# Kernel optimization log

Measured on AMD Instinct MI355X. Metric: run time of the kernel, lower is better.

Reference implementation:

```python
import jax, jax.numpy as jnp
import numpy as np
from jax import lax

B, L, D_MODEL = 4, 1024, 512
D_STATE, D_CONV, D_INNER = 16, 4, 2 * D_MODEL


def setup_inputs() -> dict:
    key = jax.random.key(0)
    ks = jax.random.split(key, 8)
    s = 0.02
    x = jax.random.normal(ks[0], (B, L, D_MODEL), dtype=jnp.float32)
    W_in = jax.random.normal(ks[1], (D_MODEL, 2 * D_INNER), dtype=jnp.float32) * s
    conv_w = jax.random.normal(ks[2], (D_INNER, 1, D_CONV), dtype=jnp.float32) * s  # OIH, depthwise
    conv_b = jnp.zeros((D_INNER,), jnp.float32)
    W_x = jax.random.normal(ks[3], (D_INNER, 2 * D_STATE), dtype=jnp.float32) * s
    W_dt = jax.random.normal(ks[4], (D_INNER, D_INNER), dtype=jnp.float32) * s
    b_dt = jnp.zeros((D_INNER,), jnp.float32)
    # A_log = -logspace(log10(0.001), log10(1.0), d_state); used directly as A in the scan
    A_log = -jnp.logspace(np.log10(1e-3), 0.0, D_STATE, dtype=jnp.float32)
    D_skip = jnp.ones((D_INNER,), jnp.float32) * 0.1
    W_out = jax.random.normal(ks[5], (D_INNER, D_MODEL), dtype=jnp.float32) * s
    gamma = jnp.ones((D_MODEL,), jnp.float32)
    beta = jnp.zeros((D_MODEL,), jnp.float32)
    return dict(x=x, W_in=W_in, conv_w=conv_w, conv_b=conv_b, W_x=W_x, W_dt=W_dt,
                b_dt=b_dt, A_log=A_log, D_skip=D_skip, W_out=W_out, gamma=gamma, beta=beta)


def _mamba_forward(x, W_in, conv_w, conv_b, W_x, W_dt, b_dt, A_log, D_skip, W_out, gamma, beta):
    x = jnp.clip(x, -10.0, 10.0)
    x_and_res = x @ W_in                                  # [B, L, 2*d_inner]
    xp, res = jnp.split(x_and_res, 2, axis=-1)
    # Depthwise causal conv1d: torch pads d_conv-1 both sides then slices [:L] -> left-pad only.
    xt = jnp.transpose(xp, (0, 2, 1))                     # [B, d_inner, L]
    xc = lax.conv_general_dilated(xt, conv_w, window_strides=(1,),
                                  padding=[(D_CONV - 1, 0)],
                                  dimension_numbers=('NCH', 'OIH', 'NCH'),
                                  feature_group_count=D_INNER)
    xc = xc + conv_b[None, :, None]
    xc = jax.nn.silu(jnp.transpose(xc, (0, 2, 1)))        # [B, L, d_inner]
    ssm = xc @ W_x                                        # [B, L, 2*d_state]
    Bm, Cm = jnp.split(ssm, 2, axis=-1)                   # each [B, L, d_state]
    delta = xc @ W_dt + b_dt                              # [B, L, d_inner] (no softplus in source)

    # Selective scan over time (sequential recurrence)
    def step(h, inp):
        u_t, d_t, B_t, C_t = inp                          # [B,I], [B,I], [B,S], [B,S]
        dA = jnp.exp(jnp.clip(d_t[:, :, None] * A_log, -5.0, 5.0))   # [B, I, S]
        h = dA * h + (d_t[:, :, None] * B_t[:, None, :]) * u_t[:, :, None]
        y = jnp.einsum('bis,bs->bi', h, C_t)
        return h, y

    tm = lambda a: jnp.swapaxes(a, 0, 1)                  # time-major
    h0 = jnp.zeros((x.shape[0], D_INNER, D_STATE), xc.dtype)
    _, ys = lax.scan(step, h0, (tm(xc), tm(delta), tm(Bm), tm(Cm)))
    y = jnp.swapaxes(ys, 0, 1) + xc * D_skip              # D skip connection

    y = y * jax.nn.silu(res)                              # gating
    out = y @ W_out
    r = out + x                                           # residual
    mu = jnp.mean(r, axis=-1, keepdims=True)
    var = jnp.var(r, axis=-1, keepdims=True)
    return gamma * (r - mu) / jnp.sqrt(var + 1e-5) + beta


def reference(x, W_in, conv_w, conv_b, W_x, W_dt, b_dt, A_log, D_skip, W_out, gamma, beta):
    return _mamba_forward(x, W_in, conv_w, conv_b, W_x, W_dt, b_dt, A_log, D_skip, W_out, gamma, beta)
```

## Files before the change

kernel.cpp:

```cpp
#include <hip/hip_runtime.h>
#include <hip/hip_bf16.h>

typedef __hip_bfloat16 bf16;
typedef unsigned short ushort_t;
typedef unsigned int uint_t;
typedef __attribute__((ext_vector_type(8))) __bf16 bf16x8;
typedef __attribute__((ext_vector_type(8))) ushort_t u16x8;
typedef __attribute__((ext_vector_type(4))) ushort_t u16x4;
typedef __attribute__((ext_vector_type(4))) float f32x4;

#define BB 4
#define LL 1024
#define DM 512
#define DS 16
#define DI 1024
#define ROWS 4096
#define NC 64
#define CT 16
#define NDTX 1152

#define CLP2 7.21347520f

__device__ __forceinline__ float b2f(bf16 v) { return __bfloat162float(v); }

__device__ __forceinline__ float load_flag(const void* src, int i, int isbf)
{
    return isbf ? b2f(((const bf16*)src)[i]) : ((const float*)src)[i];
}

__device__ __forceinline__ ushort_t f2b_bits(float v)
{
    bf16 t = __float2bfloat16(v);
    return *(ushort_t*)&t;
}

__device__ __forceinline__ float bits2f(ushort_t u)
{
    uint_t w = ((uint_t)u) << 16;
    return __uint_as_float(w);
}

__device__ __forceinline__ int detect_local(const ushort_t* wdt)
{
    __shared__ int bad;
    if (threadIdx.x == 0) bad = 0;
    __syncthreads();
    ushort_t u = wdt[threadIdx.x & 255];
    if (((u >> 7) & 0xFF) >= 127) atomicAdd(&bad, 1);
    __syncthreads();
    return (bad <= 8) ? 1 : 0;
}

__global__ __launch_bounds__(256)
void prep_all(const void* x, const void* Win, const void* Wdt, const void* Wx,
              const void* Wout, const void* cw, const void* cb, const void* Alog,
              const void* Dsk, const void* gam, const void* bet, const void* bdtin,
              bf16* __restrict__ xbf, bf16* __restrict__ WtIn,
              bf16* __restrict__ WtDtx, bf16* __restrict__ WtOut,
              float* __restrict__ ccw, float* __restrict__ ccb,
              float* __restrict__ cAlg, float* __restrict__ cDsk,
              float* __restrict__ cgam, float* __restrict__ cbet,
              float* __restrict__ bdtx)
{
    const int isbf = detect_local((const ushort_t*)Wdt);
    int blk = blockIdx.x;

    if (blk < 2048) {
        int idx = blk * 256 + threadIdx.x;
        float v[4];
        if (isbf) {
            uint2 raw = ((const uint2*)x)[idx];
            v[0] = __uint_as_float(raw.x << 16);
            v[1] = __uint_as_float(raw.x & 0xFFFF0000u);
            v[2] = __uint_as_float(raw.y << 16);
            v[3] = __uint_as_float(raw.y & 0xFFFF0000u);
        } else {
            float4 raw = ((const float4*)x)[idx];
            v[0] = raw.x; v[1] = raw.y; v[2] = raw.z; v[3] = raw.w;
        }
        uint_t b0, b1;
        b0 = f2b_bits(fminf(fmaxf(v[0], -10.f), 10.f))
           | ((uint_t)f2b_bits(fminf(fmaxf(v[1], -10.f), 10.f)) << 16);
        b1 = f2b_bits(fminf(fmaxf(v[2], -10.f), 10.f))
           | ((uint_t)f2b_bits(fminf(fmaxf(v[3], -10.f), 10.f)) << 16);
        uint2 ow; ow.x = b0; ow.y = b1;
        ((uint2*)xbf)[idx] = ow;
    } else if (blk < 4640) {
        int tb = blk - 2048;
        const void* src; bf16* dst; int K, Nsrc, tpr;
        if (tb < 1024)      { src = Win;  dst = WtIn;   K = 512;  Nsrc = 2048; tpr = 64; }
        else if (tb < 2048) { tb -= 1024; src = Wdt;  dst = WtDtx; K = 1024; Nsrc = 1024; tpr = 32; }
        else if (tb < 2080) { tb -= 2048; src = Wx;   dst = WtDtx + 1024 * 1024; K = 1024; Nsrc = 32; tpr = 1; }
        else                { tb -= 2080; src = Wout; dst = WtOut;  K = 1024; Nsrc = 512;  tpr = 16; }
        int k0 = (tb / tpr) * 32, n0 = (tb % tpr) * 32;

        __shared__ float tile[32][33];
        int tx = threadIdx.x & 31, ty = threadIdx.x >> 5;
        #pragma unroll
        for (int j = 0; j < 4; ++j)
            tile[ty + 8 * j][tx] = load_flag(src, (k0 + ty + 8 * j) * Nsrc + n0 + tx, isbf);
        __syncthreads();
        #pragma unroll
        for (int j = 0; j < 4; ++j)
            dst[(size_t)(n0 + ty + 8 * j) * K + k0 + tx] = __float2bfloat16(tile[tx][ty + 8 * j]);
    } else {
        int i = (blk - 4640) * 256 + threadIdx.x;
        if (i < 4096)        ccw[i] = load_flag(cw, i, isbf);
        else if (i < 5120)   ccb[i - 4096] = load_flag(cb, i - 4096, isbf);
        else if (i < 5136)   cAlg[i - 5120] = load_flag(Alog, i - 5120, isbf);
        else if (i < 6160)   cDsk[i - 5136] = load_flag(Dsk, i - 5136, isbf);
        else if (i < 6672)   cgam[i - 6160] = load_flag(gam, i - 6160, isbf);
        else if (i < 7184)   cbet[i - 6672] = load_flag(bet, i - 6672, isbf);
        else if (i < 8336) {
            int j = i - 7184;
            bdtx[j] = (j < DI) ? load_flag(bdtin, j, isbf) : 0.f;
        } else if (i < 106640) {
            (WtDtx + 1056 * 1024)[i - 8336] = __float2bfloat16(0.f);
        }
    }
}

__device__ __forceinline__ void gload16(const bf16* g, ushort_t* l)
{
    __builtin_amdgcn_global_load_lds(
        (const __attribute__((address_space(1))) void*)g,
        (__attribute__((address_space(3))) void*)l, 16, 0, 0);
}

template <int TM, int TN, bool OBF, bool OT, bool SPLIT>
__global__ __launch_bounds__(256)
void gemm_mfma(const bf16* __restrict__ A, const bf16* __restrict__ Bt,
               const float* __restrict__ bias, void* __restrict__ Cv,
               void* __restrict__ Cv2, int M, int N, int K)
{
    constexpr int MI = TM / 32, NJ = TN / 32;
    constexpr int NQA = TM * 8 / 256;
    constexpr int NQB = TN * 8 / 256;
    __shared__ ushort_t As[TM * 64];
    __shared__ ushort_t Bs[TN * 64];

    const int tid = threadIdx.x;
    const int lane = tid & 63;
    const int w = tid >> 6;
    const int wr = w >> 1, wc = w & 1;
    const int m0 = blockIdx.y * TM;
    const int n0 = blockIdx.x * TN;

    const bf16* gA[NQA]; ushort_t* lA[NQA];
    #pragma unroll
    for (int q = 0; q < NQA; ++q) {
        int p = q * 256 + tid;
        int row = p >> 3, kc = ((p & 7) - row) & 7;
        gA[q] = A + (size_t)(m0 + row) * K + kc * 8;
        lA[q] = &As[(q * 256 + w * 64) * 8];
    }
    const bf16* gB[NQB]; ushort_t* lB[NQB];
    #pragma unroll
    for (int q = 0; q < NQB; ++q) {
        int p = q * 256 + tid;
        int row = p >> 3, kc = ((p & 7) - row) & 7;
        gB[q] = Bt + (size_t)(n0 + row) * K + kc * 8;
        lB[q] = &Bs[(q * 256 + w * 64) * 8];
    }

    f32x4 acc[MI][NJ];
    #pragma unroll
    for (int i = 0; i < MI; ++i)
        #pragma unroll
        for (int j = 0; j < NJ; ++j)
            acc[i][j] = (f32x4){0.f, 0.f, 0.f, 0.f};

    const int ko = lane >> 4;
    const int ml = lane & 15;

    for (int k0 = 0; k0 < K; k0 += 64) {
        #pragma unroll
        for (int q = 0; q < NQA; ++q) gload16(gA[q] + k0, lA[q]);
        #pragma unroll
        for (int q = 0; q < NQB; ++q) gload16(gB[q] + k0, lB[q]);
        __syncthreads();

        #pragma unroll
        for (int half = 0; half < 2; ++half) {
            bf16x8 af[MI], bfr[NJ];
            #pragma unroll
            for (int i = 0; i < MI; ++i) {
                int m = wr * (TM / 2) + i * 16 + ml;
                af[i] = *(const bf16x8*)&As[(m * 8 + ((half * 4 + ko + m) & 7)) * 8];
            }
            #pragma unroll
            for (int j = 0; j < NJ; ++j) {
                int n = wc * (TN / 2) + j * 16 + ml;
                bfr[j] = *(const bf16x8*)&Bs[(n * 8 + ((half * 4 + ko + n) & 7)) * 8];
            }
            #pragma unroll
            for (int i = 0; i < MI; ++i)
                #pragma unroll
                for (int j = 0; j < NJ; ++j)
                    acc[i][j] = __builtin_amdgcn_mfma_f32_16x16x32_bf16(
                        af[i], bfr[j], acc[i][j], 0, 0, 0);
        }
        __syncthreads();
    }

    const int rq = lane >> 4;
    #pragma unroll
    for (int j = 0; j < NJ; ++j) {
        int n = n0 + wc * (TN / 2) + j * 16 + ml;
        float bv = bias ? bias[n] : 0.f;
        #pragma unroll
        for (int i = 0; i < MI; ++i) {
            int mb = m0 + wr * (TM / 2) + i * 16 + rq * 4;
            if (SPLIT && n >= 1024) {
                if (n < 1088) {
                    #pragma unroll
                    for (int r = 0; r < 4; ++r)
                        ((float*)Cv2)[(size_t)(mb + r) * 64 + (n - 1024)] =
                            acc[i][j][r] + bv;
                }
            } else if (OT) {
                u16x4 pk;
                #pragma unroll
                for (int r = 0; r < 4; ++r)
                    pk[r] = f2b_bits(acc[i][j][r] + bv);
                *(u16x4*)((ushort_t*)Cv + (size_t)n * M + mb) = pk;
            } else {
                #pragma unroll
                for (int r = 0; r < 4; ++r) {
                    float v = acc[i][j][r] + bv;
                    if (OBF) ((bf16*)Cv)[(size_t)(mb + r) * N + n] = __float2bfloat16(v);
                    else     ((float*)Cv)[(size_t)(mb + r) * N + n] = v;
                }
            }
        }
    }
}

__global__ __launch_bounds__(256)
void conv_silu(const bf16* __restrict__ xrbT, const float* __restrict__ cw,
               const float* __restrict__ cb, bf16* __restrict__ xcT,
               bf16* __restrict__ xc)
{
    __shared__ ushort_t tile[64 * 72];
    const int blk = blockIdx.x;
    const int ch0 = (blk & 15) * 64;
    const int T0b = (blk >> 4) * 64;
    const int lc = threadIdx.x >> 2, tg = threadIdx.x & 3;
    const int i = ch0 + lc;
    const int T0 = T0b + tg * 16;

    const ushort_t* base = (const ushort_t*)xrbT + (size_t)i * ROWS + T0;
    u16x8 m0 = *(const u16x8*)base;
    u16x8 m1 = *(const u16x8*)(base + 8);
    u16x8 pv = {0, 0, 0, 0, 0, 0, 0, 0};
    if ((T0 & (LL - 1)) != 0) pv = *(const u16x8*)(base - 8);

    float4 w = ((const float4*)cw)[i];
    float bs = cb[i];
    float xm3 = bits2f(pv[5]), xm2 = bits2f(pv[6]), xm1 = bits2f(pv[7]);
    u16x8 o0, o1;
    #pragma unroll
    for (int tt = 0; tt < 16; ++tt) {
        float x0 = bits2f(tt < 8 ? m0[tt] : m1[tt - 8]);
        float acc = bs;
        acc = fmaf(xm3, w.x, acc);
        acc = fmaf(xm2, w.y, acc);
        acc = fmaf(xm1, w.z, acc);
        acc = fmaf(x0,  w.w, acc);
        ushort_t ob = f2b_bits(acc / (1.f + __expf(-acc)));
        if (tt < 8) o0[tt] = ob; else o1[tt - 8] = ob;
        xm3 = xm2; xm2 = xm1; xm1 = x0;
    }
    ushort_t* dt = (ushort_t*)xcT + (size_t)i * ROWS + T0;
    *(u16x8*)dt = o0;
    *(u16x8*)(dt + 8) = o1;
    *(u16x8*)&tile[lc * 72 + tg * 16] = o0;
    *(u16x8*)&tile[lc * 72 + tg * 16 + 8] = o1;
    __syncthreads();
    const int lt = threadIdx.x >> 2, cg = threadIdx.x & 3;
    u16x8 q0, q1;
    #pragma unroll
    for (int j = 0; j < 8; ++j) q0[j] = tile[(cg * 16 + j) * 72 + lt];
    #pragma unroll
    for (int j = 8; j < 16; ++j) q1[j - 8] = tile[(cg * 16 + j) * 72 + lt];
    ushort_t* wp = (ushort_t*)xc + (size_t)(T0b + lt) * DI + ch0 + cg * 16;
    *(u16x8*)wp = q0;
    *(u16x8*)(wp + 8) = q1;
}

__global__ __launch_bounds__(1024)
void scan_fused(const bf16* __restrict__ xcT, const bf16* __restrict__ dT,
                const float* __restrict__ ssm, const bf16* __restrict__ xrbT,
                const float* __restrict__ A_log, const float* __restrict__ Dskip,
                bf16* __restrict__ ybf)
{
    __shared__ uint_t lsum[DS * NC * 16];

    const int tid = threadIdx.x;
    const int b = blockIdx.x >> 6;
    const int ch0 = (blockIdx.x & 63) << 4;
    const int chl = tid & 15;
    const int c = tid >> 4;
    const int i = ch0 + chl;
    const size_t tb = (size_t)b * LL + c * CT;

    float a2[DS];
    #pragma unroll
    for (int s = 0; s < DS; ++s) {
        uint_t bits = (uint_t)__builtin_amdgcn_readfirstlane((int)__float_as_uint(A_log[s]));
        a2[s] = __uint_as_float(bits) * 1.44269504f;
    }

    const u16x8* dp = (const u16x8*)((const ushort_t*)dT + (size_t)i * ROWS + tb);
    const u16x8* up = (const u16x8*)((const ushort_t*)xcT + (size_t)i * ROWS + tb);
    const u16x8* rp = (const u16x8*)((const ushort_t*)xrbT + (size_t)(1024 + i) * ROWS + tb);

    float h[DS] = {};
    float p[DS];
    #pragma unroll
    for (int s = 0; s < DS; ++s) p[s] = 1.f;

    #pragma unroll
    for (int half = 0; half < 2; ++half) {
        u16x8 dv8 = dp[half];
        u16x8 uv8 = up[half];
        #pragma unroll
        for (int t = 0; t < 8; ++t) {
            float dv = bits2f(dv8[t]);
            float uv = bits2f(uv8[t]);
            float du = dv * uv;
            const f32x4* sv = (const f32x4*)(ssm + (tb + half * 8 + t) * 64);
            #pragma unroll
            for (int g = 0; g < 4; ++g) {
                f32x4 Bq = sv[g];
                #pragma unroll
                for (int q = 0; q < 4; ++q) {
                    int s = g * 4 + q;
                    float e = fminf(fmaxf(dv * a2[s], -CLP2), CLP2);
                    float dA = exp2f(e);
                    h[s] = fmaf(dA, h[s], du * Bq[q]);
                    p[s] *= dA;
                }
            }
        }
    }
    #pragma unroll
    for (int s = 0; s < DS; ++s)
        lsum[s * 1024 + tid] = (uint_t)f2b_bits(p[s]) | ((uint_t)f2b_bits(h[s]) << 16);
    __syncthreads();

    if (tid < 256) {
        int cl = tid & 15, s = tid >> 4;
        float hh = 0.f;
        for (int cc = 0; cc < NC; ++cc) {
            int off = s * 1024 + cc * 16 + cl;
            uint_t wrd = lsum[off];
            float pp = bits2f((ushort_t)(wrd & 0xFFFF));
            float qq = bits2f((ushort_t)(wrd >> 16));
            lsum[off] = (uint_t)f2b_bits(hh);
            hh = fmaf(pp, hh, qq);
        }
    }
    __syncthreads();

    #pragma unroll
    for (int s = 0; s < DS; ++s) h[s] = bits2f((ushort_t)lsum[s * 1024 + tid]);

    const float dsk = Dskip[i];

    #pragma unroll
    for (int half = 0; half < 2; ++half) {
        u16x8 dv8 = dp[half];
        u16x8 uv8 = up[half];
        u16x8 rv8 = rp[half];
        #pragma unroll
        for (int t = 0; t < 8; ++t) {
            float dv = bits2f(dv8[t]);
            float uv = bits2f(uv8[t]);
            float du = dv * uv;
            const f32x4* sv = (const f32x4*)(ssm + (tb + half * 8 + t) * 64);
            float y = 0.f;
            #pragma unroll
            for (int g = 0; g < 4; ++g) {
                f32x4 Bq = sv[g];
                f32x4 Cq = sv[4 + g];
                #pragma unroll
                for (int q = 0; q < 4; ++q) {
                    int s = g * 4 + q;
                    float e = fminf(fmaxf(dv * a2[s], -CLP2), CLP2);
                    float dA = exp2f(e);
                    h[s] = fmaf(dA, h[s], du * Bq[q]);
                    y = fmaf(h[s], Cq[q], y);
                }
            }
            float res = bits2f(rv8[t]);
            float g2 = res / (1.f + __expf(-res));
            ybf[(tb + half * 8 + t) * DI + i] = __float2bfloat16((y + uv * dsk) * g2);
        }
    }
}

__global__ __launch_bounds__(256)
void ln_kernel(const bf16* __restrict__ outp, const void* __restrict__ xsrc,
               const void* __restrict__ wdt_probe,
               const float* __restrict__ gamma, const float* __restrict__ beta,
               void* __restrict__ out)
{
    const int isbf = detect_local((const ushort_t*)wdt_probe);
    const int row = blockIdx.x;
    const int tid = threadIdx.x;

    float r[2];
    float sum = 0.f, ss = 0.f;
    #pragma unroll
    for (int q = 0; q < 2; ++q) {
        int j = tid + q * 256;
        float xv = load_flag(xsrc, row * DM + j, isbf);
        xv = fminf(fmaxf(xv, -10.f), 10.f);
        float v = b2f(outp[(size_t)row * DM + j]) + xv;
        r[q] = v;
        sum += v;
        ss = fmaf(v, v, ss);
    }
    #pragma unroll
    for (int off = 32; off >= 1; off >>= 1) {
        sum += __shfl_down(sum, off);
        ss  += __shfl_down(ss, off);
    }
    __shared__ float s1[4], s2[4];
    __shared__ float stats[2];
    int wid = tid >> 6, lane = tid & 63;
    if (lane == 0) { s1[wid] = sum; s2[wid] = ss; }
    __syncthreads();
    if (tid == 0) {
        float S = s1[0] + s1[1] + s1[2] + s1[3];
        float Qq = s2[0] + s2[1] + s2[2] + s2[3];
        float mean = S / DM;
        float var = Qq / DM - mean * mean;
        stats[0] = mean;
        stats[1] = rsqrtf(var + 1e-5f);
    }
    __syncthreads();
    float mean = stats[0], rstd = stats[1];
    #pragma unroll
    for (int q = 0; q < 2; ++q) {
        int j = tid + q * 256;
        float v = (r[q] - mean) * rstd * gamma[j] + beta[j];
        size_t o = (size_t)row * DM + j;
        if (isbf) ((bf16*)out)[o] = __float2bfloat16(v);
        else      ((float*)out)[o] = v;
    }
}

extern "C" void kernel_launch(void* const* d_in, const int* in_sizes, int n_in,
                              void* d_out, int out_size, void* d_ws, size_t ws_size,
                              hipStream_t stream)
{
    float* W = (float*)d_ws;
    float* ccw  = W;
    float* ccb  = ccw  + 4096;
    float* cAlg = ccb  + 1024;
    float* cDsk = cAlg + 16;
    float* cgam = cDsk + 1024;
    float* cbet = cgam + 512;
    float* bdtx = cbet + 512;
    float* ssm  = bdtx + 1152;
    bf16*  xbf  = (bf16*)(ssm + 262144);
    bf16*  xrbT = xbf  + 2097152;
    bf16*  xcT  = xrbT + 8388608;
    bf16*  xc   = xcT  + 4194304;
    bf16*  ybf  = xc   + 4194304;
    bf16*  dT   = ybf  + 4194304;
    bf16*  outp = dT   + 4194304;
    bf16*  WtIn = outp + 2097152;
    bf16*  WtDtx= WtIn + 1048576;
    bf16*  WtOut= WtDtx+ 1179648;

    prep_all<<<5057, 256, 0, stream>>>(
        d_in[0], d_in[1], d_in[5], d_in[4], d_in[9], d_in[2], d_in[3],
        d_in[7], d_in[8], d_in[10], d_in[11], d_in[6],
        xbf, WtIn, WtDtx, WtOut, ccw, ccb, cAlg, cDsk, cgam, cbet, bdtx);

    gemm_mfma<128, 128, true, true, false><<<dim3(2048 / 128, ROWS / 128), 256, 0, stream>>>(
        xbf, WtIn, nullptr, xrbT, nullptr, ROWS, 2048, 512);

    conv_silu<<<1024, 256, 0, stream>>>(xrbT, ccw, ccb, xcT, xc);

    gemm_mfma<64, 128, true, true, true><<<dim3(NDTX / 128, ROWS / 64), 256, 0, stream>>>(
        xc, WtDtx, bdtx, dT, ssm, ROWS, NDTX, DI);

    scan_fused<<<256, 1024, 0, stream>>>(xcT, dT, ssm, xrbT, cAlg, cDsk, ybf);

    gemm_mfma<64, 64, true, false, false><<<dim3(DM / 64, ROWS / 64), 256, 0, stream>>>(
        ybf, WtOut, nullptr, outp, nullptr, ROWS, DM, DI);

    ln_kernel<<<ROWS, 256, 0, stream>>>(outp, d_in[0], d_in[5], cgam, cbet, d_out);
}
```

Measured before the change: 219.2 us.

## Store SSM B/C projections in bf16 and use packed float2 math in scan

The GEMM epilogue now writes the B/C state projections as bf16 instead of fp32, halving the ssm buffer that every scan thread rereads for each timestep. The scan kernel loads these as u16x8 vectors, switches from exp2f with a prescaled A to __expf with the original clip bounds, and arranges the state recurrence as float2 vectors so the compiler can emit packed FP32 instructions. The risk is lower precision in B/C and a possibly different instruction mix for the exp.

```diff
diff --git a/kernel.cpp b/kernel.cpp
--- a/kernel.cpp
+++ b/kernel.cpp
@@ -8,6 +8,7 @@
 typedef __attribute__((ext_vector_type(8))) ushort_t u16x8;
 typedef __attribute__((ext_vector_type(4))) ushort_t u16x4;
 typedef __attribute__((ext_vector_type(4))) float f32x4;
+typedef __attribute__((ext_vector_type(2))) float f32x2;
 
 #define BB 4
 #define LL 1024
@@ -18,8 +19,6 @@
 #define NC 64
 #define CT 16
 #define NDTX 1152
-
-#define CLP2 7.21347520f
 
 __device__ __forceinline__ float b2f(bf16 v) { return __bfloat162float(v); }
 
@@ -215,8 +214,8 @@
                 if (n < 1088) {
                     #pragma unroll
                     for (int r = 0; r < 4; ++r)
-                        ((float*)Cv2)[(size_t)(mb + r) * 64 + (n - 1024)] =
-                            acc[i][j][r] + bv;
+                        ((bf16*)Cv2)[(size_t)(mb + r) * 64 + (n - 1024)] =
+                            __float2bfloat16(acc[i][j][r] + bv);
                 }
             } else if (OT) {
                 u16x4 pk;
@@ -290,7 +289,7 @@
 
 __global__ __launch_bounds__(1024)
 void scan_fused(const bf16* __restrict__ xcT, const bf16* __restrict__ dT,
-                const float* __restrict__ ssm, const bf16* __restrict__ xrbT,
+                const bf16* __restrict__ ssm, const bf16* __restrict__ xrbT,
                 const float* __restrict__ A_log, const float* __restrict__ Dskip,
                 bf16* __restrict__ ybf)
 {
@@ -304,21 +303,23 @@
     const int i = ch0 + chl;
     const size_t tb = (size_t)b * LL + c * CT;
 
-    float a2[DS];
+    float a[DS];
     #pragma unroll
     for (int s = 0; s < DS; ++s) {
         uint_t bits = (uint_t)__builtin_amdgcn_readfirstlane((int)__float_as_uint(A_log[s]));
-        a2[s] = __uint_as_float(bits) * 1.44269504f;
+        a[s] = __uint_as_float(bits);
     }
 
     const u16x8* dp = (const u16x8*)((const ushort_t*)dT + (size_t)i * ROWS + tb);
     const u16x8* up = (const u16x8*)((const ushort_t*)xcT + (size_t)i * ROWS + tb);
     const u16x8* rp = (const u16x8*)((const ushort_t*)xrbT + (size_t)(1024 + i) * ROWS + tb);
 
-    float h[DS] = {};
-    float p[DS];
-    #pragma unroll
-    for (int s = 0; s < DS; ++s) p[s] = 1.f;
+    f32x2 h2[8], p2[8];
+    #pragma unroll
+    for (int k = 0; k < 8; ++k) {
+        h2[k] = (f32x2){0.f, 0.f};
+        p2[k] = (f32x2){1.f, 1.f};
+    }
 
     #pragma unroll
     for (int half = 0; half < 2; ++half) {
@@ -329,24 +330,28 @@
             float dv = bits2f(dv8[t]);
             float uv = bits2f(uv8[t]);
             float du = dv * uv;
-            const f32x4* sv = (const f32x4*)(ssm + (tb + half * 8 + t) * 64);
+            f32x2 du2 = {du, du};
+            const u16x8* sp = (const u16x8*)((const ushort_t*)ssm + (tb + half * 8 + t) * 64);
+            u16x8 B0 = sp[0], B1 = sp[1];
             #pragma unroll
-            for (int g = 0; g < 4; ++g) {
-                f32x4 Bq = sv[g];
-                #pragma unroll
-                for (int q = 0; q < 4; ++q) {
-                    int s = g * 4 + q;
-                    float e = fminf(fmaxf(dv * a2[s], -CLP2), CLP2);
-                    float dA = exp2f(e);
-                    h[s] = fmaf(dA, h[s], du * Bq[q]);
-                    p[s] *= dA;
-                }
+            for (int k = 0; k < 8; ++k) {
+                float eA = fminf(fmaxf(dv * a[2 * k],     -5.f), 5.f);
+                float eB = fminf(fmaxf(dv * a[2 * k + 1], -5.f), 5.f);
+                f32x2 dA = {__expf(eA), __expf(eB)};
+                f32x2 Bv = {bits2f(k < 4 ? B0[2 * k] : B1[2 * k - 8]),
+                            bits2f(k < 4 ? B0[2 * k + 1] : B1[2 * k - 7])};
+                h2[k] = dA * h2[k] + du2 * Bv;
+                p2[k] = p2[k] * dA;
             }
         }
     }
     #pragma unroll
-    for (int s = 0; s < DS; ++s)
-        lsum[s * 1024 + tid] = (uint_t)f2b_bits(p[s]) | ((uint_t)f2b_bits(h[s]) << 16);
+    for (int k = 0; k < 8; ++k) {
+        lsum[(2 * k) * 1024 + tid] =
+            (uint_t)f2b_bits(p2[k][0]) | ((uint_t)f2b_bits(h2[k][0]) << 16);
+        lsum[(2 * k + 1) * 1024 + tid] =
+            (uint_t)f2b_bits(p2[k][1]) | ((uint_t)f2b_bits(h2[k][1]) << 16);
+    }
     __syncthreads();
 
     if (tid < 256) {
@@ -364,7 +369,10 @@
     __syncthreads();
 
     #pragma unroll
-    for (int s = 0; s < DS; ++s) h[s] = bits2f((ushort_t)lsum[s * 1024 + tid]);
+    for (int k = 0; k < 8; ++k) {
+        h2[k][0] = bits2f((ushort_t)lsum[(2 * k) * 1024 + tid]);
+        h2[k][1] = bits2f((ushort_t)lsum[(2 * k + 1) * 1024 + tid]);
+    }
 
     const float dsk = Dskip[i];
 
@@ -378,24 +386,26 @@
             float dv = bits2f(dv8[t]);
             float uv = bits2f(uv8[t]);
             float du = dv * uv;
-            const f32x4* sv = (const f32x4*)(ssm + (tb + half * 8 + t) * 64);
-            float y = 0.f;
+            f32x2 du2 = {du, du};
+            const u16x8* sp = (const u16x8*)((const ushort_t*)ssm + (tb + half * 8 + t) * 64);
+            u16x8 B0 = sp[0], B1 = sp[1], C0 = sp[2], C1 = sp[3];
+            f32x2 y2 = {0.f, 0.f};
             #pragma unroll
-            for (int g = 0; g < 4; ++g) {
-                f32x4 Bq = sv[g];
-                f32x4 Cq = sv[4 + g];
-                #pragma unroll
-                for (int q = 0; q < 4; ++q) {
-                    int s = g * 4 + q;
-                    float e = fminf(fmaxf(dv * a2[s], -CLP2), CLP2);
-                    float dA = exp2f(e);
-                    h[s] = fmaf(dA, h[s], du * Bq[q]);
-                    y = fmaf(h[s], Cq[q], y);
-                }
+            for (int k = 0; k < 8; ++k) {
+                float eA = fminf(fmaxf(dv * a[2 * k],     -5.f), 5.f);
+                float eB = fminf(fmaxf(dv * a[2 * k + 1], -5.f), 5.f);
+                f32x2 dA = {__expf(eA), __expf(eB)};
+                f32x2 Bv = {bits2f(k < 4 ? B0[2 * k] : B1[2 * k - 8]),
+                            bits2f(k < 4 ? B0[2 * k + 1] : B1[2 * k - 7])};
+                f32x2 Cv = {bits2f(k < 4 ? C0[2 * k] : C1[2 * k - 8]),
+                            bits2f(k < 4 ? C0[2 * k + 1] : C1[2 * k - 7])};
+                h2[k] = dA * h2[k] + du2 * Bv;
+                y2 = y2 + h2[k] * Cv;
             }
+            float y = y2[0] + y2[1];
             float res = bits2f(rv8[t]);
-            float g2 = res / (1.f + __expf(-res));
-            ybf[(tb + half * 8 + t) * DI + i] = __float2bfloat16((y + uv * dsk) * g2);
+            float g = res / (1.f + __expf(-res));
+            ybf[(tb + half * 8 + t) * DI + i] = __float2bfloat16((y + uv * dsk) * g);
         }
     }
 }
@@ -464,14 +474,14 @@
     float* cgam = cDsk + 1024;
     float* cbet = cgam + 512;
     float* bdtx = cbet + 512;
-    float* ssm  = bdtx + 1152;
-    bf16*  xbf  = (bf16*)(ssm + 262144);
+    bf16*  xbf  = (bf16*)(bdtx + 1152);
     bf16*  xrbT = xbf  + 2097152;
     bf16*  xcT  = xrbT + 8388608;
     bf16*  xc   = xcT  + 4194304;
     bf16*  ybf  = xc   + 4194304;
     bf16*  dT   = ybf  + 4194304;
-    bf16*  outp = dT   + 4194304;
+    bf16*  ssm  = dT   + 4194304;
+    bf16*  outp = ssm  + 262144;
     bf16*  WtIn = outp + 2097152;
     bf16*  WtDtx= WtIn + 1048576;
     bf16*  WtOut= WtDtx+ 1179648;
```

Measured after the change: 206.4 us (median of 2 runs). 1.06x faster.
